# Kernel optimization log

Hardware: AMD Instinct MI355X
Metric: run time of the kernel (lower is better)

The kernel has to match this reference:

```python
import jax, jax.numpy as jnp
import numpy as np

B, S, D, E, K = 4, 4096, 2048, 64, 2


def setup_inputs() -> dict:
    key = jax.random.key(0)
    k1, k2 = jax.random.split(key)
    hidden_states = jax.random.normal(k1, (B, S, D), dtype=jnp.float32)
    gate_weight = jax.random.normal(k2, (E, D), dtype=jnp.float32) * 0.02
    return {"hidden_states": hidden_states, "gate_weight": gate_weight}


def reference(hidden_states, gate_weight):
    b, s, d = hidden_states.shape
    e = gate_weight.shape[0]
    n = b * s
    x = hidden_states.reshape(n, d)
    logits = x @ gate_weight.T                                  # [N, E]
    # Original reassigns gate_logits = softmax(gate_logits) in fp32.
    probs = jax.nn.softmax(logits.astype(jnp.float32), axis=-1)  # [N, E]

    top_v, top_i = jax.lax.top_k(probs, K)                       # [N, K]
    top_k_gates = top_v  # normalize_gate_prob_before_dropping=False

    oh = jax.nn.one_hot(top_i, e, dtype=probs.dtype)             # [N, K, E]
    gates = jnp.einsum('nke,nk->ne', oh, top_k_gates)            # scatter of top-k gates

    # Auxiliary losses (training path, use_aux_loss=True)
    gates_mean = gates.mean(axis=0)                              # [E]
    selection_mean = oh.sum(axis=(0, 1)) / n                     # [E]
    load_balancing_loss = (gates_mean * selection_mean).sum() * e
    # NOTE: original computes z-loss on the softmaxed probs (gate_logits was overwritten)
    router_z_loss = (jax.nn.logsumexp(probs, axis=-1) ** 2).mean()

    # torch scatter_ with index [B,S,1,1] only ever writes slot k=0.
    dispatch0 = oh.sum(axis=1).reshape(b, s, e)                  # 1.0 at top-k experts
    combine0 = gates.reshape(b, s, e)
    pad = ((0, 0), (0, 0), (0, 0), (0, K - 1))
    dispatch_tensor = jnp.pad(dispatch0[..., None], pad)         # [B,S,E,K]
    combine_tensor = jnp.pad(combine0[..., None], pad)           # [B,S,E,K]

    return dispatch_tensor, combine_tensor, load_balancing_loss, router_z_loss
```

## Files before the change

kernel.cpp:

```cpp
#include <hip/hip_runtime.h>
#include <hip/hip_bf16.h>
#include <cstddef>

namespace {
constexpr int kD = 2048;
constexpr int kE = 64;
constexpr int kN = 16384;
constexpr size_t kDispatchFloats = (size_t)kN * kE * 2;
constexpr size_t kWsplitOff = 1024;
}

typedef short short8_t __attribute__((ext_vector_type(8)));
typedef float f32x4 __attribute__((ext_vector_type(4)));

__device__ __forceinline__ void split2(float f, unsigned short& s1,
                                       unsigned short& s2) {
  __hip_bfloat16 h1 = __float2bfloat16(f);
  float r1 = f - __bfloat162float(h1);
  __hip_bfloat16 h2 = __float2bfloat16(r1);
  s1 = __builtin_bit_cast(unsigned short, h1);
  s2 = __builtin_bit_cast(unsigned short, h2);
}

__device__ __forceinline__ void split8_2(f32x4 a, f32x4 b, short8_t& o1,
                                         short8_t& o2) {
  unsigned short s1, s2;
#define SP(v, i, j) \
  split2((v)[i], s1, s2); o1[j] = (short)s1; o2[j] = (short)s2;
  SP(a, 0, 0) SP(a, 1, 1) SP(a, 2, 2) SP(a, 3, 3)
  SP(b, 0, 4) SP(b, 1, 5) SP(b, 2, 6) SP(b, 3, 7)
#undef SP
}

__global__ __launch_bounds__(256)
void prep_kernel(const float* __restrict__ W, unsigned short* __restrict__ img,
                 float* __restrict__ ws) {
  const int t = blockIdx.x * 256 + threadIdx.x;
  if (t < 512) ws[t] = 0.0f;
  const int g   = t >> 9;
  const int row = (t >> 3) & 63;
  const int cs8 = t & 7;
  const int co  = cs8 ^ (row & 7);
  const float* src = W + (size_t)row * kD + g * 64 + co * 8;
  const float4 v0 = *reinterpret_cast<const float4*>(src);
  const float4 v1 = *reinterpret_cast<const float4*>(src + 4);
  short8_t o1, o2;
  unsigned short s1, s2;
  split2(v0.x, s1, s2); o1[0]=(short)s1; o2[0]=(short)s2;
  split2(v0.y, s1, s2); o1[1]=(short)s1; o2[1]=(short)s2;
  split2(v0.z, s1, s2); o1[2]=(short)s1; o2[2]=(short)s2;
  split2(v0.w, s1, s2); o1[3]=(short)s1; o2[3]=(short)s2;
  split2(v1.x, s1, s2); o1[4]=(short)s1; o2[4]=(short)s2;
  split2(v1.y, s1, s2); o1[5]=(short)s1; o2[5]=(short)s2;
  split2(v1.z, s1, s2); o1[6]=(short)s1; o2[6]=(short)s2;
  split2(v1.w, s1, s2); o1[7]=(short)s1; o2[7]=(short)s2;
  unsigned short* dst = img + (size_t)g * 8192 + row * 64 + cs8 * 8;
  *reinterpret_cast<short8_t*>(dst + 0 * 4096) = o1;
  *reinterpret_cast<short8_t*>(dst + 1 * 4096) = o2;
}

__global__ __launch_bounds__(512, 6)
void moe_kernel(const float* __restrict__ x,
                const unsigned short* __restrict__ wimg,
                float* __restrict__ out, float* __restrict__ ws) {
  __shared__ __attribute__((aligned(16))) unsigned char smem[49152];
  float* xsf = reinterpret_cast<float*>(smem);
  unsigned short (*wt)[2][64][64] =
      reinterpret_cast<unsigned short (*)[2][64][64]>(smem + 16384);
  float (*lg)[65] = reinterpret_cast<float (*)[65]>(smem);
  __shared__ int ti0[32], ti1[32];
  __shared__ float tv0[32], tv1[32], tz2[32];

  const int tid  = threadIdx.x;
  const int lane = tid & 63;
  const int wv   = __builtin_amdgcn_readfirstlane(tid >> 6);
  const int th   = wv >> 2;
  const int wc   = (wv >> 1) & 1;
  const int kh   = wv & 1;
  const int tile = blockIdx.x;
  const int lrow = lane & 15;
  const int lk   = lane >> 4;

  const int row = tid >> 4, t16 = tid & 15;
  const float4* __restrict__ bx = reinterpret_cast<const float4*>(x) +
      ((size_t)tile * 32 + row) * 512 + t16 * 2;
  const unsigned short* __restrict__ wbase = wimg + tid * 8;
  unsigned short* wtf = &wt[0][0][0][0];
  const int su0 = ((2 * t16) ^ (row & 31)) * 4;
  const int su1 = ((2 * t16 + 1) ^ (row & 31)) * 4;

  f32x4 acc[2];
  const f32x4 z4 = {0.0f, 0.0f, 0.0f, 0.0f};
  acc[0] = z4; acc[1] = z4;

  float4 vx0 = bx[0], vx1 = bx[1];

  for (int c = 0; c < 16; ++c) {
    const unsigned short* wsrc = wbase + (size_t)(2 * c) * 8192;
#pragma unroll
    for (int i = 0; i < 4; ++i)
      __builtin_amdgcn_global_load_lds(
          (const __attribute__((address_space(1))) void*)(wsrc + i * 4096),
          (__attribute__((address_space(3))) void*)(wtf + i * 4096 + wv * 512),
          16, 0, 0);
    __builtin_amdgcn_sched_barrier(0);
    const float4 xa = vx0, xb = vx1;
    const int cn = (c + 1) & 15;
    vx0 = bx[cn * 32 + 0];
    vx1 = bx[cn * 32 + 1];
    *reinterpret_cast<float4*>(xsf + row * 128 + su0) = xa;
    *reinterpret_cast<float4*>(xsf + row * 128 + su1) = xb;
    asm volatile("s_waitcnt vmcnt(2) lgkmcnt(0)" ::: "memory");
    __builtin_amdgcn_sched_barrier(0);
    __builtin_amdgcn_s_barrier();
    __builtin_amdgcn_sched_barrier(0);
    __builtin_amdgcn_s_setprio(1);
#pragma unroll
    for (int ks = 0; ks < 2; ++ks) {
      const int kc = ks * 4 + lk;
      short8_t b1[2], b2[2];
#pragma unroll
      for (int nt = 0; nt < 2; ++nt) {
        const int e = wc * 32 + nt * 16 + lrow;
        const int cw = (kc ^ (e & 7)) * 8;
        b1[nt] = *reinterpret_cast<const short8_t*>(&wt[kh][0][e][cw]);
        b2[nt] = *reinterpret_cast<const short8_t*>(&wt[kh][1][e][cw]);
      }
      const int ra = th * 16 + lrow;
      const int u0 = kh * 16 + ks * 8 + 2 * lk;
      const int ca0 = ((u0) ^ (ra & 31)) * 4;
      const int ca1 = ((u0 + 1) ^ (ra & 31)) * 4;
      const f32x4 va = *reinterpret_cast<const f32x4*>(xsf + ra * 128 + ca0);
      const f32x4 vb = *reinterpret_cast<const f32x4*>(xsf + ra * 128 + ca1);
      short8_t a1, a2;
      split8_2(va, vb, a1, a2);
#pragma unroll
      for (int nt = 0; nt < 2; ++nt) {
        acc[nt] = __builtin_amdgcn_mfma_f32_16x16x32_bf16(a1, b1[nt], acc[nt], 0, 0, 0);
        acc[nt] = __builtin_amdgcn_mfma_f32_16x16x32_bf16(a1, b2[nt], acc[nt], 0, 0, 0);
        acc[nt] = __builtin_amdgcn_mfma_f32_16x16x32_bf16(a2, b1[nt], acc[nt], 0, 0, 0);
      }
    }
    __builtin_amdgcn_s_setprio(0);
    __builtin_amdgcn_sched_barrier(0);
    __builtin_amdgcn_s_barrier();
  }

  if (kh == 1) {
#pragma unroll
    for (int nt = 0; nt < 2; ++nt)
#pragma unroll
      for (int r = 0; r < 4; ++r)
        lg[th * 16 + lk * 4 + r][wc * 32 + nt * 16 + lrow] = acc[nt][r];
  }
  __syncthreads();
  if (kh == 0) {
#pragma unroll
    for (int nt = 0; nt < 2; ++nt)
#pragma unroll
      for (int r = 0; r < 4; ++r) {
        const int t = th * 16 + lk * 4 + r;
        const int e = wc * 32 + nt * 16 + lrow;
        lg[t][e] += acc[nt][r];
      }
  }
  __syncthreads();

  if (tid < 32) {
    float v0 = -INFINITY, v1 = -INFINITY;
    int i0 = 0, i1 = 0;
    for (int e = 0; e < kE; ++e) {
      const float l = lg[tid][e];
      if (l > v0) { v1 = v0; i1 = i0; v0 = l; i0 = e; }
      else if (l > v1) { v1 = l; i1 = e; }
    }
    const float m = v0;
    float s = 0.0f;
    for (int e = 0; e < kE; ++e) s += __expf(lg[tid][e] - m);
    const float rs = 1.0f / s;
    float zexp = 0.0f;
    for (int e = 0; e < kE; ++e) zexp += __expf(__expf(lg[tid][e] - m) * rs);
    const float z = logf(zexp);
    ti0[tid] = i0; ti1[tid] = i1;
    tv0[tid] = rs;
    tv1[tid] = __expf(v1 - m) * rs;
    tz2[tid] = z * z;
  }
  __syncthreads();

  if (tid < kE) {
    float g = 0.0f, cnt = 0.0f;
    for (int t = 0; t < 32; ++t) {
      if (ti0[t] == tid) { g += tv0[t]; cnt += 1.0f; }
      if (ti1[t] == tid) { g += tv1[t]; cnt += 1.0f; }
    }
    atomicAdd(&ws[tid], g);
    atomicAdd(&ws[kE + tid], cnt);
  }
  if (tid < 32) {
    float z2 = tz2[tid];
    z2 += __shfl_down(z2, 16);
    z2 += __shfl_down(z2, 8);
    z2 += __shfl_down(z2, 4);
    z2 += __shfl_down(z2, 2);
    z2 += __shfl_down(z2, 1);
    if (tid == 0) atomicAdd(&ws[2 * kE], z2);
  }

  {
    const int t = tid >> 4, sub = tid & 15;
    const int i0 = ti0[t], i1 = ti1[t];
    const float v0 = tv0[t], v1 = tv1[t];
    const size_t n = (size_t)tile * 32 + t;
    float4* __restrict__ dp = reinterpret_cast<float4*>(out) + n * 32;
    float4* __restrict__ cp =
        reinterpret_cast<float4*>(out) + kDispatchFloats / 4 + n * 32;
#pragma unroll
    for (int j = 0; j < 2; ++j) {
      const int qq = sub * 2 + j;
      const int e0 = qq * 2, e1 = qq * 2 + 1;
      const float d0v = (e0 == i0 || e0 == i1) ? 1.0f : 0.0f;
      const float d1v = (e1 == i0 || e1 == i1) ? 1.0f : 0.0f;
      const float c0 = (e0 == i0) ? v0 : ((e0 == i1) ? v1 : 0.0f);
      const float c1 = (e1 == i0) ? v0 : ((e1 == i1) ? v1 : 0.0f);
      dp[qq] = make_float4(d0v, 0.0f, d1v, 0.0f);
      cp[qq] = make_float4(c0, 0.0f, c1, 0.0f);
    }
  }
}

__global__ void finalize_kernel(const float* __restrict__ ws,
                                float* __restrict__ out) {
  const int e = threadIdx.x;
  float prod = ws[e] * ws[kE + e];
  for (int off = 32; off; off >>= 1) prod += __shfl_down(prod, off);
  if (e == 0) {
    const size_t base = kDispatchFloats * 2;
    const float invN = 1.0f / (float)kN;
    out[base]     = prod * ((float)kE * invN * invN);
    out[base + 1] = ws[2 * kE] * invN;
  }
}

extern "C" void kernel_launch(void* const* d_in, const int* in_sizes, int n_in,
                              void* d_out, int out_size, void* d_ws,
                              size_t ws_size, hipStream_t stream) {
  const float* x = (const float*)d_in[0];
  const float* W = (const float*)d_in[1];
  float* out = (float*)d_out;
  float* ws = (float*)d_ws;
  unsigned short* wimg = (unsigned short*)(ws + kWsplitOff);

  prep_kernel<<<64, 256, 0, stream>>>(W, wimg, ws);
  moe_kernel<<<512, 512, 0, stream>>>(x, wimg, out, ws);
  finalize_kernel<<<1, kE, 0, stream>>>(ws, out);
}
```

Measured before the change: 65.48 us.

## Double-buffer weight tiles in LDS and load x directly into registers

Restructures the main GEMM loop so the bf16 weight tiles are double-buffered in shared memory. The next chunk's global-to-LDS load is issued right after a single barrier per iteration, replacing the old two barriers. Activation rows are now loaded straight into MFMA operand registers with a one-chunk register prefetch, removing the LDS staging and swizzled stores for x. This doubles LDS use to 64KB and lowers the occupancy hint from 6 to 4 waves. It also waits for all outstanding loads (vmcnt 0) at the top of each iteration, which may limit how much latency is actually hidden.

```diff
diff --git a/kernel.cpp b/kernel.cpp
--- a/kernel.cpp
+++ b/kernel.cpp
@@ -59,14 +59,13 @@
   *reinterpret_cast<short8_t*>(dst + 1 * 4096) = o2;
 }
 
-__global__ __launch_bounds__(512, 6)
+__global__ __launch_bounds__(512, 4)
 void moe_kernel(const float* __restrict__ x,
                 const unsigned short* __restrict__ wimg,
                 float* __restrict__ out, float* __restrict__ ws) {
-  __shared__ __attribute__((aligned(16))) unsigned char smem[49152];
-  float* xsf = reinterpret_cast<float*>(smem);
-  unsigned short (*wt)[2][64][64] =
-      reinterpret_cast<unsigned short (*)[2][64][64]>(smem + 16384);
+  __shared__ __attribute__((aligned(16))) unsigned char smem[65536];
+  unsigned short (*wt)[2][2][64][64] =
+      reinterpret_cast<unsigned short (*)[2][2][64][64]>(smem);
   float (*lg)[65] = reinterpret_cast<float (*)[65]>(smem);
   __shared__ int ti0[32], ti1[32];
   __shared__ float tv0[32], tv1[32], tz2[32];
@@ -81,39 +80,56 @@
   const int lrow = lane & 15;
   const int lk   = lane >> 4;
 
-  const int row = tid >> 4, t16 = tid & 15;
-  const float4* __restrict__ bx = reinterpret_cast<const float4*>(x) +
-      ((size_t)tile * 32 + row) * 512 + t16 * 2;
+  const float* __restrict__ xb =
+      x + (size_t)(tile * 32 + th * 16 + lrow) * kD + kh * 64 + lk * 8;
   const unsigned short* __restrict__ wbase = wimg + tid * 8;
-  unsigned short* wtf = &wt[0][0][0][0];
-  const int su0 = ((2 * t16) ^ (row & 31)) * 4;
-  const int su1 = ((2 * t16 + 1) ^ (row & 31)) * 4;
+  unsigned short* wtf = reinterpret_cast<unsigned short*>(smem);
 
   f32x4 acc[2];
   const f32x4 z4 = {0.0f, 0.0f, 0.0f, 0.0f};
   acc[0] = z4; acc[1] = z4;
 
-  float4 vx0 = bx[0], vx1 = bx[1];
-
-  for (int c = 0; c < 16; ++c) {
-    const unsigned short* wsrc = wbase + (size_t)(2 * c) * 8192;
+  f32x4 xc0, xc1, xc2, xc3, xn0, xn1, xn2, xn3;
+
+  {
 #pragma unroll
     for (int i = 0; i < 4; ++i)
       __builtin_amdgcn_global_load_lds(
-          (const __attribute__((address_space(1))) void*)(wsrc + i * 4096),
+          (const __attribute__((address_space(1))) void*)(wbase + i * 4096),
           (__attribute__((address_space(3))) void*)(wtf + i * 4096 + wv * 512),
           16, 0, 0);
-    __builtin_amdgcn_sched_barrier(0);
-    const float4 xa = vx0, xb = vx1;
+    xc0 = *reinterpret_cast<const f32x4*>(xb);
+    xc1 = *reinterpret_cast<const f32x4*>(xb + 4);
+    xc2 = *reinterpret_cast<const f32x4*>(xb + 32);
+    xc3 = *reinterpret_cast<const f32x4*>(xb + 36);
+  }
+
+#pragma unroll 2
+  for (int c = 0; c < 16; ++c) {
+    const int cb = c & 1;
     const int cn = (c + 1) & 15;
-    vx0 = bx[cn * 32 + 0];
-    vx1 = bx[cn * 32 + 1];
-    *reinterpret_cast<float4*>(xsf + row * 128 + su0) = xa;
-    *reinterpret_cast<float4*>(xsf + row * 128 + su1) = xb;
-    asm volatile("s_waitcnt vmcnt(2) lgkmcnt(0)" ::: "memory");
+    asm volatile("s_waitcnt vmcnt(0) lgkmcnt(0)" ::: "memory");
     __builtin_amdgcn_sched_barrier(0);
     __builtin_amdgcn_s_barrier();
     __builtin_amdgcn_sched_barrier(0);
+    {
+      const unsigned short* wsrc = wbase + (size_t)(2 * cn) * 8192;
+      unsigned short* dst = wtf + (cb ^ 1) * 16384;
+#pragma unroll
+      for (int i = 0; i < 4; ++i)
+        __builtin_amdgcn_global_load_lds(
+            (const __attribute__((address_space(1))) void*)(wsrc + i * 4096),
+            (__attribute__((address_space(3))) void*)(dst + i * 4096 + wv * 512),
+            16, 0, 0);
+    }
+    {
+      const float* p = xb + (size_t)cn * 128;
+      xn0 = *reinterpret_cast<const f32x4*>(p);
+      xn1 = *reinterpret_cast<const f32x4*>(p + 4);
+      xn2 = *reinterpret_cast<const f32x4*>(p + 32);
+      xn3 = *reinterpret_cast<const f32x4*>(p + 36);
+    }
+    __builtin_amdgcn_sched_barrier(0);
     __builtin_amdgcn_s_setprio(1);
 #pragma unroll
     for (int ks = 0; ks < 2; ++ks) {
@@ -123,17 +139,12 @@
       for (int nt = 0; nt < 2; ++nt) {
         const int e = wc * 32 + nt * 16 + lrow;
         const int cw = (kc ^ (e & 7)) * 8;
-        b1[nt] = *reinterpret_cast<const short8_t*>(&wt[kh][0][e][cw]);
-        b2[nt] = *reinterpret_cast<const short8_t*>(&wt[kh][1][e][cw]);
+        b1[nt] = *reinterpret_cast<const short8_t*>(&wt[cb][kh][0][e][cw]);
+        b2[nt] = *reinterpret_cast<const short8_t*>(&wt[cb][kh][1][e][cw]);
       }
-      const int ra = th * 16 + lrow;
-      const int u0 = kh * 16 + ks * 8 + 2 * lk;
-      const int ca0 = ((u0) ^ (ra & 31)) * 4;
-      const int ca1 = ((u0 + 1) ^ (ra & 31)) * 4;
-      const f32x4 va = *reinterpret_cast<const f32x4*>(xsf + ra * 128 + ca0);
-      const f32x4 vb = *reinterpret_cast<const f32x4*>(xsf + ra * 128 + ca1);
       short8_t a1, a2;
-      split8_2(va, vb, a1, a2);
+      if (ks == 0) split8_2(xc0, xc1, a1, a2);
+      else         split8_2(xc2, xc3, a1, a2);
 #pragma unroll
       for (int nt = 0; nt < 2; ++nt) {
         acc[nt] = __builtin_amdgcn_mfma_f32_16x16x32_bf16(a1, b1[nt], acc[nt], 0, 0, 0);
@@ -142,10 +153,10 @@
       }
     }
     __builtin_amdgcn_s_setprio(0);
-    __builtin_amdgcn_sched_barrier(0);
-    __builtin_amdgcn_s_barrier();
-  }
-
+    xc0 = xn0; xc1 = xn1; xc2 = xn2; xc3 = xn3;
+  }
+
+  __syncthreads();
   if (kh == 1) {
 #pragma unroll
     for (int nt = 0; nt < 2; ++nt)
```

Measured after the change: 68.69 us. 4.9% more time.
